# Performance work log

Hardware: AMD Instinct MI355X
Metric: run time of the kernel (lower is better)

The kernel has to match this reference:

```python
import jax, jax.numpy as jnp
import numpy as np

V, D, B, L = 1_000_000, 128, 16384, 50  # vocab, embed_dim, num_bags, bag_len
N = B * L  # total indices


def setup_inputs() -> dict:
    key = jax.random.key(0)
    k0, k1, k2, k3 = jax.random.split(key, 4)
    # int4-packed table: each byte holds two 4-bit codes (low nibble = even elem)
    weights = jax.random.randint(k0, (V, D // 2), 0, 256, dtype=jnp.int32)
    scales = jax.random.uniform(k1, (V,), jnp.float32, 0.01, 0.1)  # per-row scale
    zeros = jax.random.randint(k2, (V,), 0, 16).astype(jnp.float32)  # per-row zero-point
    indices = jax.random.randint(k3, (N,), 0, V, dtype=jnp.int32)
    offsets = jnp.arange(B + 1, dtype=jnp.int32) * L  # include_last_offset=True
    other_tensor = jax.random.normal(jax.random.fold_in(key, 7), (B, D), jnp.float32)
    return {"weights": weights, "scales": scales, "zeros": zeros,
            "indices": indices, "offsets": offsets, "other_tensor": other_tensor}


def _quant_embedding_bag(weights, scales, zeros, indices, offsets):
    n = indices.shape[0]
    wq = weights[indices]                      # [N, D//2] packed bytes (gather)
    low = wq & 0xF
    high = (wq >> 4) & 0xF
    q = jnp.stack([low, high], axis=-1).reshape(n, D)  # [N, D] int4 codes
    deq = (q.astype(jnp.float32) - zeros[indices][:, None]) * scales[indices][:, None]
    # bag id per index from offsets (include_last_offset -> offsets has B+1 entries)
    seg = jnp.clip(jnp.searchsorted(offsets, jnp.arange(n, dtype=offsets.dtype),
                                    side="right") - 1, 0, B - 1)
    return jax.ops.segment_sum(deq, seg, num_segments=B)  # mode=0 (sum)


def reference(weights, scales, zeros, indices, offsets, other_tensor):
    eb = _quant_embedding_bag(weights, scales, zeros, indices, offsets)
    # eb1 == eb2 (identical calls in the original module); other_tensor_pos=-1, cat_dim=1
    return jnp.concatenate([eb, eb, other_tensor], axis=1)
```

## Files before the change

### kernel.cpp

```cpp
#include <hip/hip_runtime.h>


#define DIM 128
#define DPR 64

__global__ __launch_bounds__(256) void qebag_kernel(
    const unsigned* __restrict__ weights,
    const float* __restrict__ scales,
    const float* __restrict__ zeros,
    const int* __restrict__ indices,
    const int* __restrict__ offsets,
    const float* __restrict__ other,
    float* __restrict__ out,
    int B) {
  const int wave = threadIdx.x >> 6;
  const int lane = threadIdx.x & 63;
  int bag = blockIdx.x * 4 + wave;
  if (bag >= B) return;
  bag = __builtin_amdgcn_readfirstlane(bag);

  const int start = offsets[bag];
  const int count = offsets[bag + 1] - start;

  float acc_lo = 0.f, acc_hi = 0.f, corr = 0.f;

  for (int base = 0; base < count; base += 64) {
    const int cnt = min(64, count - base);

    int idx = 0;
    float s = 0.f, sz = 0.f;
    if (lane < cnt) {
      idx = indices[start + base + lane];
      s = scales[idx];
      sz = s * zeros[idx];
    }
    float c = sz;
    #pragma unroll
    for (int off = 1; off < 64; off <<= 1) c += __shfl_xor(c, off);
    corr += c;

    #pragma unroll 5
    for (int j = 0; j < cnt; ++j) {
      const int ij = __builtin_amdgcn_readlane(idx, j);
      const float sj =
          __uint_as_float(__builtin_amdgcn_readlane(__float_as_uint(s), j));
      const unsigned w = weights[(size_t)ij * DPR + lane];
      acc_lo = fmaf(sj, (float)(w & 0xFu), acc_lo);
      acc_hi = fmaf(sj, (float)((w >> 4) & 0xFu), acc_hi);
    }
  }

  const float2 e = make_float2(acc_lo - corr, acc_hi - corr);
  float2* orow = (float2*)(out + (size_t)bag * (3 * DIM));
  const float2* oth = (const float2*)(other + (size_t)bag * DIM);
  orow[lane]       = e;
  orow[64 + lane]  = e;
  orow[128 + lane] = oth[lane];
}

extern "C" void kernel_launch(void* const* d_in, const int* in_sizes, int n_in,
                              void* d_out, int out_size, void* d_ws, size_t ws_size,
                              hipStream_t stream) {
  const unsigned* weights = (const unsigned*)d_in[0];
  const float* scales     = (const float*)d_in[1];
  const float* zeros      = (const float*)d_in[2];
  const int* indices      = (const int*)d_in[3];
  const int* offsets      = (const int*)d_in[4];
  const float* other      = (const float*)d_in[5];
  float* out              = (float*)d_out;

  const int B = in_sizes[5] / DIM;
  const int blocks = (B + 3) / 4;

  qebag_kernel<<<blocks, 256, 0, stream>>>(weights, scales, zeros, indices,
                                           offsets, other, out, B);
}
```

Measured before the change: 380.1 us.

## Gather four embedding rows per wave with 16-byte loads per lane

Each wave now splits into four 16-lane groups. Each group fetches a different embedding row, and every lane loads a uint4 (8 int4 codes) instead of one 32-bit word. Partial sums are reduced across the groups with xor shuffles, and the output is written with float4 stores. The goal is fewer loop iterations and wider loads, so more gather requests are in flight per wave and the latency-bound random row fetches are hidden better. The cost is 8 accumulators per lane, an extra cross-group reduction, and a few wasted loads of row 0 when the bag length is not a multiple of 4.

```diff
diff --git a/kernel.cpp b/kernel.cpp
--- a/kernel.cpp
+++ b/kernel.cpp
@@ -2,10 +2,9 @@
 
 
 #define DIM 128
-#define DPR 64
 
 __global__ __launch_bounds__(256) void qebag_kernel(
-    const unsigned* __restrict__ weights,
+    const uint4* __restrict__ weights,
     const float* __restrict__ scales,
     const float* __restrict__ zeros,
     const int* __restrict__ indices,
@@ -15,6 +14,8 @@
     int B) {
   const int wave = threadIdx.x >> 6;
   const int lane = threadIdx.x & 63;
+  const int g = lane >> 4;
+  const int t = lane & 15;
   int bag = blockIdx.x * 4 + wave;
   if (bag >= B) return;
   bag = __builtin_amdgcn_readfirstlane(bag);
@@ -22,13 +23,15 @@
   const int start = offsets[bag];
   const int count = offsets[bag + 1] - start;
 
-  float acc_lo = 0.f, acc_hi = 0.f, corr = 0.f;
+  float acc[8];
+  #pragma unroll
+  for (int k = 0; k < 8; ++k) acc[k] = 0.f;
+  float corr = 0.f;
 
   for (int base = 0; base < count; base += 64) {
     const int cnt = min(64, count - base);
 
-    int idx = 0;
-    float s = 0.f, sz = 0.f;
+    int idx = 0; float s = 0.f, sz = 0.f;
     if (lane < cnt) {
       idx = indices[start + base + lane];
       s = scales[idx];
@@ -39,35 +42,54 @@
     for (int off = 1; off < 64; off <<= 1) c += __shfl_xor(c, off);
     corr += c;
 
-    #pragma unroll 5
-    for (int j = 0; j < cnt; ++j) {
-      const int ij = __builtin_amdgcn_readlane(idx, j);
-      const float sj =
-          __uint_as_float(__builtin_amdgcn_readlane(__float_as_uint(s), j));
-      const unsigned w = weights[(size_t)ij * DPR + lane];
-      acc_lo = fmaf(sj, (float)(w & 0xFu), acc_lo);
-      acc_hi = fmaf(sj, (float)((w >> 4) & 0xFu), acc_hi);
+    const int iters = (cnt + 3) >> 2;
+    #pragma unroll 4
+    for (int i = 0; i < iters; ++i) {
+      const int src = 4 * i + g;
+      const int ij = __shfl(idx, src);
+      const float sj = __shfl(s, src);
+      const uint4 w = weights[(size_t)ij * 16 + t];
+      acc[0] = fmaf(sj, (float)(w.x & 0xFu), acc[0]);
+      acc[1] = fmaf(sj, (float)((w.x >> 4) & 0xFu), acc[1]);
+      acc[2] = fmaf(sj, (float)(w.y & 0xFu), acc[2]);
+      acc[3] = fmaf(sj, (float)((w.y >> 4) & 0xFu), acc[3]);
+      acc[4] = fmaf(sj, (float)(w.z & 0xFu), acc[4]);
+      acc[5] = fmaf(sj, (float)((w.z >> 4) & 0xFu), acc[5]);
+      acc[6] = fmaf(sj, (float)(w.w & 0xFu), acc[6]);
+      acc[7] = fmaf(sj, (float)((w.w >> 4) & 0xFu), acc[7]);
     }
   }
 
-  const float2 e = make_float2(acc_lo - corr, acc_hi - corr);
-  float2* orow = (float2*)(out + (size_t)bag * (3 * DIM));
-  const float2* oth = (const float2*)(other + (size_t)bag * DIM);
-  orow[lane]       = e;
-  orow[64 + lane]  = e;
-  orow[128 + lane] = oth[lane];
+  #pragma unroll
+  for (int k = 0; k < 8; ++k) {
+    acc[k] += __shfl_xor(acc[k], 16);
+    acc[k] += __shfl_xor(acc[k], 32);
+    acc[k] -= corr;
+  }
+
+  float4* o4 = (float4*)(out + (size_t)bag * (3 * DIM));
+  if (g < 2) {
+    const float4 lo = make_float4(acc[0], acc[1], acc[2], acc[3]);
+    const float4 hi = make_float4(acc[4], acc[5], acc[6], acc[7]);
+    o4[g * 32 + 2 * t]     = lo;
+    o4[g * 32 + 2 * t + 1] = hi;
+  } else {
+    const int h = (g - 2) * 16 + t;
+    const float4* oth = (const float4*)(other + (size_t)bag * DIM);
+    o4[64 + h] = oth[h];
+  }
 }
 
 extern "C" void kernel_launch(void* const* d_in, const int* in_sizes, int n_in,
                               void* d_out, int out_size, void* d_ws, size_t ws_size,
                               hipStream_t stream) {
-  const unsigned* weights = (const unsigned*)d_in[0];
-  const float* scales     = (const float*)d_in[1];
-  const float* zeros      = (const float*)d_in[2];
-  const int* indices      = (const int*)d_in[3];
-  const int* offsets      = (const int*)d_in[4];
-  const float* other      = (const float*)d_in[5];
-  float* out              = (float*)d_out;
+  const uint4* weights  = (const uint4*)d_in[0];
+  const float* scales   = (const float*)d_in[1];
+  const float* zeros    = (const float*)d_in[2];
+  const int* indices    = (const int*)d_in[3];
+  const int* offsets    = (const int*)d_in[4];
+  const float* other    = (const float*)d_in[5];
+  float* out            = (float*)d_out;
 
   const int B = in_sizes[5] / DIM;
   const int blocks = (B + 3) / 4;
```

After: 356.9 us. -6.1%, faster.
